# Kernel optimization log

Hardware: AMD Instinct MI355X
Metric: run time of the kernel (lower is better)

The kernel has to match this reference:

```python
import jax, jax.numpy as jnp
import numpy as np
from jax import lax

B, H, G, T = 16384, 128, 5, 12

def setup_inputs() -> dict:
    key = jax.random.key(0)
    ks = jax.random.split(key, 12)
    s = 0.05  # weight scale for numerical sanity
    return {
        "encoder_hidden": jax.random.normal(ks[0], (B, H), jnp.float32),
        "encoder_cell": jax.random.normal(ks[1], (B, H), jnp.float32),
        "last_position": jax.random.normal(ks[2], (B, 2), jnp.float32),
        "gp_w1": jax.random.normal(ks[3], (H, H), jnp.float32) * s,
        "gp_b1": jnp.zeros((H,), jnp.float32),
        "gp_w2": jax.random.normal(ks[4], (H, G * 2), jnp.float32) * s,
        "gp_b2": jnp.zeros((G * 2,), jnp.float32),
        "pr_w1": jax.random.normal(ks[5], (H, H // 2), jnp.float32) * s,
        "pr_b1": jnp.zeros((H // 2,), jnp.float32),
        "pr_w2": jax.random.normal(ks[6], (H // 2, G), jnp.float32) * s,
        "pr_b2": jnp.zeros((G,), jnp.float32),
        "w_ih": jax.random.normal(ks[7], (4, 4 * H), jnp.float32) * s,   # LSTM input weights [in=4, 4H] (i,f,g,o)
        "w_hh": jax.random.normal(ks[8], (H, 4 * H), jnp.float32) * s,   # LSTM recurrent weights [H, 4H]
        "b_ih": jnp.zeros((4 * H,), jnp.float32),
        "b_hh": jnp.zeros((4 * H,), jnp.float32),
        "ph_w": jax.random.normal(ks[9], (H, 2), jnp.float32) * s,
        "ph_b": jnp.zeros((2,), jnp.float32),
    }

def reference(encoder_hidden, encoder_cell, last_position,
              gp_w1, gp_b1, gp_w2, gp_b2,
              pr_w1, pr_b1, pr_w2, pr_b2,
              w_ih, w_hh, b_ih, b_hh, ph_w, ph_b):
    b = encoder_hidden.shape[0]
    # goal prediction: residual on last_position
    g_hid = jax.nn.relu(encoder_hidden @ gp_w1 + gp_b1)
    goals = (g_hid @ gp_w2 + gp_b2).reshape(b, G, 2) + last_position[:, None, :]  # [B,G,2]
    # goal probabilities
    p_hid = jax.nn.relu(encoder_hidden @ pr_w1 + pr_b1)
    goal_probs = jax.nn.softmax(p_hid @ pr_w2 + pr_b2, axis=-1)  # [B,G]
    # batch all goals together: leading goal dim [G,B,...]
    goals_gb = jnp.swapaxes(goals, 0, 1)                      # [G,B,2]
    h0 = jnp.broadcast_to(encoder_hidden, (G, b, H))
    c0 = jnp.broadcast_to(encoder_cell, (G, b, H))
    pos0 = jnp.broadcast_to(last_position, (G, b, 2))
    bias = b_ih + b_hh

    def step(carry, _):
        pos, h, c = carry
        x = jnp.concatenate([pos, goals_gb], axis=-1)          # [G,B,4]
        gates = x @ w_ih + h @ w_hh + bias                      # [G,B,4H]
        i, f, g, o = jnp.split(gates, 4, axis=-1)
        c_new = jax.nn.sigmoid(f) * c + jax.nn.sigmoid(i) * jnp.tanh(g)
        h_new = jax.nn.sigmoid(o) * jnp.tanh(c_new)
        pos_new = pos + (h_new @ ph_w + ph_b)                   # residual position update
        return (pos_new, h_new, c_new), pos_new

    _, path = lax.scan(step, (pos0, h0, c0), None, length=T)   # [T,G,B,2]
    predictions = jnp.transpose(path, (2, 1, 0, 3))            # [B,G,T,2]
    return predictions, goals, goal_probs
```

## Files before the change

### kernel.cpp

```cpp
#include <hip/hip_runtime.h>

#define Bn 16384
#define Hn 128
#define Gn 5
#define Tn 12

typedef __attribute__((ext_vector_type(8))) __bf16 bf16x8;
typedef __attribute__((ext_vector_type(4))) float f32x4;
typedef __attribute__((ext_vector_type(4))) unsigned int u32x4;
typedef __attribute__((ext_vector_type(2))) unsigned int u32x2;
typedef unsigned int u32;
typedef unsigned short u16;

#define MFMA(a, b, c) __builtin_amdgcn_mfma_f32_16x16x32_bf16((a), (b), (c), 0, 0, 0)

__device__ __forceinline__ u16 f2bf(float f) { return __builtin_bit_cast(u16, (__bf16)f); }
__device__ __forceinline__ u32 pk2(float a, float b) { return (u32)f2bf(a) | ((u32)f2bf(b) << 16); }

__device__ __forceinline__ int hbsw(int row, int bytein) {
    return row * 256 + ((((bytein >> 4) ^ row) & 15) << 4) + (bytein & 15);
}
__device__ __forceinline__ int pbsw(int row, int bytein) {
    return row * 128 + ((((bytein >> 4) ^ row) & 7) << 4) + (bytein & 15);
}

__global__ __launch_bounds__(256) void k_phaseA(
    const float* __restrict__ eh, const float* __restrict__ lastpos,
    const float* __restrict__ gp_w1, const float* __restrict__ gp_b1,
    const float* __restrict__ gp_w2, const float* __restrict__ gp_b2,
    const float* __restrict__ pr_w1, const float* __restrict__ pr_b1,
    const float* __restrict__ pr_w2, const float* __restrict__ pr_b2,
    float* __restrict__ goals_o, float* __restrict__ probs_o)
{
    __shared__ __align__(16) char eT[64 * 256];
    __shared__ __align__(16) char gT[64 * 256];
    __shared__ __align__(16) char pT[64 * 128];
    __shared__ float lgT[64 * 8];

    const int tid = threadIdx.x;
    const int lane = tid & 63;
    const int wv = tid >> 6;
    const int lg = lane >> 4, li = lane & 15;
    const int r0 = blockIdx.x * 64;
    const int rowbase = wv * 16;

    {
        int row = tid >> 2, seg = tid & 3;
        const float* src = eh + (size_t)(r0 + row) * Hn + seg * 32;
#pragma unroll
        for (int cc = 0; cc < 4; ++cc) {
            u32 p0 = pk2(src[cc * 8 + 0], src[cc * 8 + 1]);
            u32 p1 = pk2(src[cc * 8 + 2], src[cc * 8 + 3]);
            u32 p2 = pk2(src[cc * 8 + 4], src[cc * 8 + 5]);
            u32 p3 = pk2(src[cc * 8 + 6], src[cc * 8 + 7]);
            *(u32x4*)(eT + hbsw(row, seg * 64 + cc * 16)) = (u32x4){p0, p1, p2, p3};
        }
    }
    __syncthreads();

    bf16x8 Ae[4];
#pragma unroll
    for (int kc = 0; kc < 4; ++kc)
        Ae[kc] = *(const bf16x8*)(eT + hbsw(rowbase + li, kc * 64 + lg * 16));

#pragma unroll 1
    for (int nt = 0; nt < 8; ++nt) {
        int c1 = nt * 16 + li;
        f32x4 acc = {0.f, 0.f, 0.f, 0.f};
#pragma unroll
        for (int kc = 0; kc < 4; ++kc) {
            bf16x8 bfr;
#pragma unroll
            for (int j = 0; j < 8; ++j)
                bfr[j] = (__bf16)gp_w1[(size_t)(kc * 32 + lg * 8 + j) * Hn + c1];
            acc = MFMA(Ae[kc], bfr, acc);
        }
        float bias = gp_b1[c1];
#pragma unroll
        for (int r = 0; r < 4; ++r) {
            int row = rowbase + lg * 4 + r;
            float v = fmaxf(acc[r] + bias, 0.f);
            *(u16*)(gT + hbsw(row, c1 * 2)) = f2bf(v);
        }
    }
    __syncthreads();

    {
        bf16x8 Ag[4];
#pragma unroll
        for (int kc = 0; kc < 4; ++kc)
            Ag[kc] = *(const bf16x8*)(gT + hbsw(rowbase + li, kc * 64 + lg * 16));
        f32x4 acc = {0.f, 0.f, 0.f, 0.f};
#pragma unroll
        for (int kc = 0; kc < 4; ++kc) {
            bf16x8 bfr;
#pragma unroll
            for (int j = 0; j < 8; ++j) {
                int k = kc * 32 + lg * 8 + j;
                bfr[j] = (li < 10) ? (__bf16)gp_w2[k * 10 + li] : (__bf16)0.f;
            }
            acc = MFMA(Ag[kc], bfr, acc);
        }
        if (li < 10) {
            float b2 = gp_b2[li];
#pragma unroll
            for (int r = 0; r < 4; ++r) {
                int b = r0 + rowbase + lg * 4 + r;
                float v = acc[r] + b2 + lastpos[(size_t)b * 2 + (li & 1)];
                goals_o[(size_t)b * 10 + li] = v;
            }
        }
    }

#pragma unroll 1
    for (int nt = 0; nt < 4; ++nt) {
        int c1 = nt * 16 + li;
        f32x4 acc = {0.f, 0.f, 0.f, 0.f};
#pragma unroll
        for (int kc = 0; kc < 4; ++kc) {
            bf16x8 bfr;
#pragma unroll
            for (int j = 0; j < 8; ++j)
                bfr[j] = (__bf16)pr_w1[(size_t)(kc * 32 + lg * 8 + j) * 64 + c1];
            acc = MFMA(Ae[kc], bfr, acc);
        }
        float bias = pr_b1[c1];
#pragma unroll
        for (int r = 0; r < 4; ++r) {
            int row = rowbase + lg * 4 + r;
            float v = fmaxf(acc[r] + bias, 0.f);
            *(u16*)(pT + pbsw(row, c1 * 2)) = f2bf(v);
        }
    }
    __syncthreads();

    {
        bf16x8 Ap[2];
#pragma unroll
        for (int kc = 0; kc < 2; ++kc)
            Ap[kc] = *(const bf16x8*)(pT + pbsw(rowbase + li, kc * 64 + lg * 16));
        f32x4 acc = {0.f, 0.f, 0.f, 0.f};
#pragma unroll
        for (int kc = 0; kc < 2; ++kc) {
            bf16x8 bfr;
#pragma unroll
            for (int j = 0; j < 8; ++j) {
                int k = kc * 32 + lg * 8 + j;
                bfr[j] = (li < 5) ? (__bf16)pr_w2[k * 5 + li] : (__bf16)0.f;
            }
            acc = MFMA(Ap[kc], bfr, acc);
        }
        if (li < 5) {
            float b2 = pr_b2[li];
#pragma unroll
            for (int r = 0; r < 4; ++r) {
                int row = rowbase + lg * 4 + r;
                lgT[row * 8 + li] = acc[r] + b2;
            }
        }
    }
    __syncthreads();

    if (tid < 64) {
        int row = tid;
        float v0 = lgT[row * 8 + 0], v1 = lgT[row * 8 + 1], v2 = lgT[row * 8 + 2];
        float v3 = lgT[row * 8 + 3], v4 = lgT[row * 8 + 4];
        float mx = fmaxf(fmaxf(fmaxf(v0, v1), fmaxf(v2, v3)), v4);
        float e0 = __builtin_amdgcn_exp2f((v0 - mx) * 1.44269504f);
        float e1 = __builtin_amdgcn_exp2f((v1 - mx) * 1.44269504f);
        float e2 = __builtin_amdgcn_exp2f((v2 - mx) * 1.44269504f);
        float e3 = __builtin_amdgcn_exp2f((v3 - mx) * 1.44269504f);
        float e4 = __builtin_amdgcn_exp2f((v4 - mx) * 1.44269504f);
        float rs = __builtin_amdgcn_rcpf(e0 + e1 + e2 + e3 + e4);
        size_t ob = (size_t)(r0 + row) * 5;
        probs_o[ob + 0] = e0 * rs;
        probs_o[ob + 1] = e1 * rs;
        probs_o[ob + 2] = e2 * rs;
        probs_o[ob + 3] = e3 * rs;
        probs_o[ob + 4] = e4 * rs;
    }
}

__global__ __launch_bounds__(512) void k_lstm(
    const float* __restrict__ eh, const float* __restrict__ ec,
    const float* __restrict__ lastpos,
    const float* __restrict__ w_ih, const float* __restrict__ w_hh,
    const float* __restrict__ b_ih, const float* __restrict__ b_hh,
    const float* __restrict__ ph_w, const float* __restrict__ ph_b,
    const float* __restrict__ goals_o, float* __restrict__ preds)
{
#define MT 10
#define ROWS (MT * 16)
#define BUFB (ROWS * 256)
    __shared__ __align__(16) char hT[2][BUFB];

    const int tid = threadIdx.x;
    const int lane = tid & 63;
    const int wv = tid >> 6;
    const int lg = lane >> 4, li = lane & 15;
    const int r0 = blockIdx.x * ROWS;

    const float NL = -1.44269504f;
    const float PG = 2.88539008f;

    bf16x8 Wh[4][4];
    bf16x8 Wx[4];
#pragma unroll
    for (int gt = 0; gt < 4; ++gt) {
        const float s = (gt == 2) ? PG : NL;
        const int cg = gt * 128 + wv * 16 + li;
#pragma unroll
        for (int kc = 0; kc < 4; ++kc) {
            bf16x8 f;
#pragma unroll
            for (int j = 0; j < 8; ++j)
                f[j] = (__bf16)(w_hh[(size_t)(kc * 32 + lg * 8 + j) * 512 + cg] * s);
            Wh[gt][kc] = f;
        }
        bf16x8 fx;
#pragma unroll
        for (int j = 0; j < 8; ++j) {
            int k = lg * 8 + j;
            float v = 0.f;
            if (k < 4) v = w_ih[k * 512 + cg] * s;
            else if (k == 4) v = (b_ih[cg] + b_hh[cg]) * s;
            fx[j] = (__bf16)v;
        }
        Wx[gt] = fx;
    }

    bf16x8 php[4];
#pragma unroll
    for (int kc = 0; kc < 4; ++kc) {
        u32 w[4];
#pragma unroll
        for (int jp = 0; jp < 4; ++jp) {
            int k = kc * 32 + lg * 8 + jp * 2;
            u32 xw = pk2(ph_w[k * 2 + 0], ph_w[k * 2 + 2]);
            u32 yw = pk2(ph_w[k * 2 + 1], ph_w[k * 2 + 3]);
            w[jp] = (li == 0) ? xw : yw;
        }
        php[kc] = __builtin_bit_cast(bf16x8, (u32x4){w[0], w[1], w[2], w[3]});
    }
    const float phb0 = ph_b[0], phb1 = ph_b[1];

    u32 gpk[MT];
    float px[MT], py[MT];
#pragma unroll
    for (int m = 0; m < MT; ++m) {
        int gr = r0 + m * 16 + li;
        float2 g2 = *(const float2*)(goals_o + (size_t)gr * 2);
        gpk[m] = pk2(g2.x, g2.y);
        float2 p = *(const float2*)(lastpos + (size_t)(gr / 5) * 2);
        px[m] = p.x; py[m] = p.y;
    }

    const int ro0 = hbsw(li, 0 + lg * 16);
    const int ro1 = hbsw(li, 64 + lg * 16);
    const int ro2 = hbsw(li, 128 + lg * 16);
    const int ro3 = hbsw(li, 192 + lg * 16);
    const int wo  = hbsw(li, wv * 32 + lg * 8);

#pragma unroll
    for (int it = 0; it < 5; ++it) {
        int chunk = tid + it * 512;
        int row = chunk >> 4, seg = chunk & 15;
        const float* src = eh + (size_t)((r0 + row) / 5) * Hn + seg * 8;
        u32 p0 = pk2(src[0], src[1]);
        u32 p1 = pk2(src[2], src[3]);
        u32 p2 = pk2(src[4], src[5]);
        u32 p3 = pk2(src[6], src[7]);
        *(u32x4*)(hT[0] + hbsw(row, seg * 16)) = (u32x4){p0, p1, p2, p3};
    }

    f32x4 c[MT];
#pragma unroll
    for (int m = 0; m < MT; ++m) {
        int b = (r0 + m * 16 + li) / 5;
        float4 cv = *(const float4*)(ec + (size_t)b * Hn + wv * 16 + lg * 4);
        c[m] = (f32x4){cv.x, cv.y, cv.z, cv.w};
    }

    __syncthreads();

#pragma unroll 1
    for (int t = 0; t < Tn; ++t) {
        const char* rbp = hT[0] + (t & 1) * BUFB;
        char* wbp = hT[0] + ((t & 1) ^ 1) * BUFB;
#pragma unroll
        for (int m = 0; m < MT; ++m) {
            const int mo = m * 4096;
            bf16x8 H0 = *(const bf16x8*)(rbp + ro0 + mo);
            bf16x8 H1 = *(const bf16x8*)(rbp + ro1 + mo);
            bf16x8 H2 = *(const bf16x8*)(rbp + ro2 + mo);
            bf16x8 H3 = *(const bf16x8*)(rbp + ro3 + mo);

            f32x4 a0 = {0.f, 0.f, 0.f, 0.f}, a1 = {0.f, 0.f, 0.f, 0.f};
            f32x4 a2 = {0.f, 0.f, 0.f, 0.f}, a3 = {0.f, 0.f, 0.f, 0.f};
            a0 = MFMA(Wh[0][0], H0, a0); a1 = MFMA(Wh[1][0], H0, a1);
            a2 = MFMA(Wh[2][0], H0, a2); a3 = MFMA(Wh[3][0], H0, a3);
            a0 = MFMA(Wh[0][1], H1, a0); a1 = MFMA(Wh[1][1], H1, a1);
            a2 = MFMA(Wh[2][1], H1, a2); a3 = MFMA(Wh[3][1], H1, a3);
            a0 = MFMA(Wh[0][2], H2, a0); a1 = MFMA(Wh[1][2], H2, a1);
            a2 = MFMA(Wh[2][2], H2, a2); a3 = MFMA(Wh[3][2], H2, a3);
            a0 = MFMA(Wh[0][3], H3, a0); a1 = MFMA(Wh[1][3], H3, a1);
            a2 = MFMA(Wh[2][3], H3, a2); a3 = MFMA(Wh[3][3], H3, a3);

            if (t > 0) {
                f32x4 pacc = {0.f, 0.f, 0.f, 0.f};
                pacc = MFMA(php[0], H0, pacc);
                pacc = MFMA(php[1], H1, pacc);
                pacc = MFMA(php[2], H2, pacc);
                pacc = MFMA(php[3], H3, pacc);
                px[m] += pacc[0] + phb0;
                py[m] += pacc[1] + phb1;
                if (((m & 7) == wv) && lg == 0) {
                    size_t o = ((size_t)(r0 + m * 16 + li) * Tn + (t - 1)) * 2;
                    *(float2*)(preds + o) = make_float2(px[m], py[m]);
                }
            }

            bf16x8 xf = __builtin_bit_cast(bf16x8,
                (u32x4){pk2(px[m], py[m]), gpk[m], 0x00003F80u, 0u});
            a0 = MFMA(Wx[0], xf, a0);
            a1 = MFMA(Wx[1], xf, a1);
            a2 = MFMA(Wx[2], xf, a2);
            a3 = MFMA(Wx[3], xf, a3);

            u32 w0, w1;
            {
                float hvv[4];
#pragma unroll
                for (int r = 0; r < 4; ++r) {
                    float si = __builtin_amdgcn_rcpf(1.0f + __builtin_amdgcn_exp2f(a0[r]));
                    float sf = __builtin_amdgcn_rcpf(1.0f + __builtin_amdgcn_exp2f(a1[r]));
                    float tg = 1.0f - 2.0f * __builtin_amdgcn_rcpf(1.0f + __builtin_amdgcn_exp2f(a2[r]));
                    float so = __builtin_amdgcn_rcpf(1.0f + __builtin_amdgcn_exp2f(a3[r]));
                    float cn = sf * c[m][r] + si * tg;
                    c[m][r] = cn;
                    float tc = 1.0f - 2.0f * __builtin_amdgcn_rcpf(1.0f + __builtin_amdgcn_exp2f(PG * cn));
                    hvv[r] = so * tc;
                }
                w0 = pk2(hvv[0], hvv[1]);
                w1 = pk2(hvv[2], hvv[3]);
            }
            *(u32x2*)(wbp + wo + mo) = (u32x2){w0, w1};
        }
        __syncthreads();
    }

#pragma unroll
    for (int m = 0; m < MT; ++m) {
        if ((m & 7) != wv) continue;
        const char* rbp = hT[0];
        const int mo = m * 4096;
        bf16x8 H0 = *(const bf16x8*)(rbp + ro0 + mo);
        bf16x8 H1 = *(const bf16x8*)(rbp + ro1 + mo);
        bf16x8 H2 = *(const bf16x8*)(rbp + ro2 + mo);
        bf16x8 H3 = *(const bf16x8*)(rbp + ro3 + mo);
        f32x4 pacc = {0.f, 0.f, 0.f, 0.f};
        pacc = MFMA(php[0], H0, pacc);
        pacc = MFMA(php[1], H1, pacc);
        pacc = MFMA(php[2], H2, pacc);
        pacc = MFMA(php[3], H3, pacc);
        if (lg == 0) {
            float fx = px[m] + pacc[0] + phb0;
            float fy = py[m] + pacc[1] + phb1;
            size_t o = ((size_t)(r0 + m * 16 + li) * Tn + (Tn - 1)) * 2;
            *(float2*)(preds + o) = make_float2(fx, fy);
        }
    }
#undef MT
#undef ROWS
#undef BUFB
}

extern "C" void kernel_launch(void* const* d_in, const int* in_sizes, int n_in,
                              void* d_out, int out_size, void* d_ws, size_t ws_size,
                              hipStream_t stream)
{
    (void)in_sizes; (void)n_in; (void)out_size; (void)d_ws; (void)ws_size;
    const float* eh   = (const float*)d_in[0];
    const float* ec   = (const float*)d_in[1];
    const float* lp   = (const float*)d_in[2];
    const float* gpw1 = (const float*)d_in[3];
    const float* gpb1 = (const float*)d_in[4];
    const float* gpw2 = (const float*)d_in[5];
    const float* gpb2 = (const float*)d_in[6];
    const float* prw1 = (const float*)d_in[7];
    const float* prb1 = (const float*)d_in[8];
    const float* prw2 = (const float*)d_in[9];
    const float* prb2 = (const float*)d_in[10];
    const float* wih  = (const float*)d_in[11];
    const float* whh  = (const float*)d_in[12];
    const float* bih  = (const float*)d_in[13];
    const float* bhh  = (const float*)d_in[14];
    const float* phw  = (const float*)d_in[15];
    const float* phb  = (const float*)d_in[16];

    float* out = (float*)d_out;
    float* preds = out;
    float* goals = out + (size_t)Bn * Gn * Tn * 2;
    float* probs = out + (size_t)Bn * Gn * Tn * 2 + (size_t)Bn * Gn * 2;

    k_phaseA<<<Bn / 64, 256, 0, stream>>>(eh, lp, gpw1, gpb1, gpw2, gpb2,
                                          prw1, prb1, prw2, prb2, goals, probs);
    k_lstm<<<(Bn * Gn) / 160, 512, 0, stream>>>(eh, ec, lp, wih, whh, bih, bhh,
                                                phw, phb, goals, preds);
}
```

Baseline: 246.5 us.

## Double LSTM rows per block with single h buffer and shared position state

```diff
diff --git a/kernel.cpp b/kernel.cpp
--- a/kernel.cpp
+++ b/kernel.cpp
@@ -181,7 +181,7 @@
     }
 }
 
-__global__ __launch_bounds__(512) void k_lstm(
+__global__ __launch_bounds__(512, 2) void k_lstm(
     const float* __restrict__ eh, const float* __restrict__ ec,
     const float* __restrict__ lastpos,
     const float* __restrict__ w_ih, const float* __restrict__ w_hh,
@@ -189,10 +189,12 @@
     const float* __restrict__ ph_w, const float* __restrict__ ph_b,
     const float* __restrict__ goals_o, float* __restrict__ preds)
 {
-#define MT 10
+#define MT 20
 #define ROWS (MT * 16)
 #define BUFB (ROWS * 256)
-    __shared__ __align__(16) char hT[2][BUFB];
+    __shared__ __align__(16) char hT[BUFB];
+    __shared__ float2 posb[2][ROWS];
+    __shared__ u32 gpkT[ROWS];
 
     const int tid = threadIdx.x;
     const int lane = tid & 63;
@@ -244,17 +246,6 @@
     }
     const float phb0 = ph_b[0], phb1 = ph_b[1];
 
-    u32 gpk[MT];
-    float px[MT], py[MT];
-#pragma unroll
-    for (int m = 0; m < MT; ++m) {
-        int gr = r0 + m * 16 + li;
-        float2 g2 = *(const float2*)(goals_o + (size_t)gr * 2);
-        gpk[m] = pk2(g2.x, g2.y);
-        float2 p = *(const float2*)(lastpos + (size_t)(gr / 5) * 2);
-        px[m] = p.x; py[m] = p.y;
-    }
-
     const int ro0 = hbsw(li, 0 + lg * 16);
     const int ro1 = hbsw(li, 64 + lg * 16);
     const int ro2 = hbsw(li, 128 + lg * 16);
@@ -262,7 +253,7 @@
     const int wo  = hbsw(li, wv * 32 + lg * 8);
 
 #pragma unroll
-    for (int it = 0; it < 5; ++it) {
+    for (int it = 0; it < 10; ++it) {
         int chunk = tid + it * 512;
         int row = chunk >> 4, seg = chunk & 15;
         const float* src = eh + (size_t)((r0 + row) / 5) * Hn + seg * 8;
@@ -270,7 +261,15 @@
         u32 p1 = pk2(src[2], src[3]);
         u32 p2 = pk2(src[4], src[5]);
         u32 p3 = pk2(src[6], src[7]);
-        *(u32x4*)(hT[0] + hbsw(row, seg * 16)) = (u32x4){p0, p1, p2, p3};
+        *(u32x4*)(hT + hbsw(row, seg * 16)) = (u32x4){p0, p1, p2, p3};
+    }
+    if (tid < ROWS) {
+        int gr = r0 + tid;
+        float2 p = *(const float2*)(lastpos + (size_t)(gr / 5) * 2);
+        posb[0][tid] = p;
+        posb[1][tid] = p;
+        float2 g2 = *(const float2*)(goals_o + (size_t)gr * 2);
+        gpkT[tid] = pk2(g2.x, g2.y);
     }
 
     f32x4 c[MT];
@@ -285,15 +284,16 @@
 
 #pragma unroll 1
     for (int t = 0; t < Tn; ++t) {
-        const char* rbp = hT[0] + (t & 1) * BUFB;
-        char* wbp = hT[0] + ((t & 1) ^ 1) * BUFB;
-#pragma unroll
-        for (int m = 0; m < MT; ++m) {
+        const float2* posR = posb[t & 1];
+        float2* posW = posb[(t & 1) ^ 1];
+        u32 hnA[10], hnB[10];
+
+        auto compute = [&](int m, int i) {
             const int mo = m * 4096;
-            bf16x8 H0 = *(const bf16x8*)(rbp + ro0 + mo);
-            bf16x8 H1 = *(const bf16x8*)(rbp + ro1 + mo);
-            bf16x8 H2 = *(const bf16x8*)(rbp + ro2 + mo);
-            bf16x8 H3 = *(const bf16x8*)(rbp + ro3 + mo);
+            bf16x8 H0 = *(const bf16x8*)(hT + ro0 + mo);
+            bf16x8 H1 = *(const bf16x8*)(hT + ro1 + mo);
+            bf16x8 H2 = *(const bf16x8*)(hT + ro2 + mo);
+            bf16x8 H3 = *(const bf16x8*)(hT + ro3 + mo);
 
             f32x4 a0 = {0.f, 0.f, 0.f, 0.f}, a1 = {0.f, 0.f, 0.f, 0.f};
             f32x4 a2 = {0.f, 0.f, 0.f, 0.f}, a3 = {0.f, 0.f, 0.f, 0.f};
@@ -306,66 +306,79 @@
             a0 = MFMA(Wh[0][3], H3, a0); a1 = MFMA(Wh[1][3], H3, a1);
             a2 = MFMA(Wh[2][3], H3, a2); a3 = MFMA(Wh[3][3], H3, a3);
 
+            float2 pp = posR[m * 16 + li];
+            float pxv = pp.x, pyv = pp.y;
             if (t > 0) {
                 f32x4 pacc = {0.f, 0.f, 0.f, 0.f};
                 pacc = MFMA(php[0], H0, pacc);
                 pacc = MFMA(php[1], H1, pacc);
                 pacc = MFMA(php[2], H2, pacc);
                 pacc = MFMA(php[3], H3, pacc);
-                px[m] += pacc[0] + phb0;
-                py[m] += pacc[1] + phb1;
-                if (((m & 7) == wv) && lg == 0) {
+                pxv += pacc[0] + phb0;
+                pyv += pacc[1] + phb1;
+                if (wv == 0 && lg == 0) {
+                    posW[m * 16 + li] = make_float2(pxv, pyv);
                     size_t o = ((size_t)(r0 + m * 16 + li) * Tn + (t - 1)) * 2;
-                    *(float2*)(preds + o) = make_float2(px[m], py[m]);
+                    *(float2*)(preds + o) = make_float2(pxv, pyv);
                 }
             }
 
+            u32 gk = gpkT[m * 16 + li];
             bf16x8 xf = __builtin_bit_cast(bf16x8,
-                (u32x4){pk2(px[m], py[m]), gpk[m], 0x00003F80u, 0u});
+                (u32x4){pk2(pxv, pyv), gk, 0x00003F80u, 0u});
             a0 = MFMA(Wx[0], xf, a0);
             a1 = MFMA(Wx[1], xf, a1);
             a2 = MFMA(Wx[2], xf, a2);
             a3 = MFMA(Wx[3], xf, a3);
 
-            u32 w0, w1;
-            {
-                float hvv[4];
-#pragma unroll
-                for (int r = 0; r < 4; ++r) {
-                    float si = __builtin_amdgcn_rcpf(1.0f + __builtin_amdgcn_exp2f(a0[r]));
-                    float sf = __builtin_amdgcn_rcpf(1.0f + __builtin_amdgcn_exp2f(a1[r]));
-                    float tg = 1.0f - 2.0f * __builtin_amdgcn_rcpf(1.0f + __builtin_amdgcn_exp2f(a2[r]));
-                    float so = __builtin_amdgcn_rcpf(1.0f + __builtin_amdgcn_exp2f(a3[r]));
-                    float cn = sf * c[m][r] + si * tg;
-                    c[m][r] = cn;
-                    float tc = 1.0f - 2.0f * __builtin_amdgcn_rcpf(1.0f + __builtin_amdgcn_exp2f(PG * cn));
-                    hvv[r] = so * tc;
-                }
-                w0 = pk2(hvv[0], hvv[1]);
-                w1 = pk2(hvv[2], hvv[3]);
-            }
-            *(u32x2*)(wbp + wo + mo) = (u32x2){w0, w1};
-        }
+            float hvv[4];
+#pragma unroll
+            for (int r = 0; r < 4; ++r) {
+                float si = __builtin_amdgcn_rcpf(1.0f + __builtin_amdgcn_exp2f(a0[r]));
+                float sf = __builtin_amdgcn_rcpf(1.0f + __builtin_amdgcn_exp2f(a1[r]));
+                float tg = 1.0f - 2.0f * __builtin_amdgcn_rcpf(1.0f + __builtin_amdgcn_exp2f(a2[r]));
+                float so = __builtin_amdgcn_rcpf(1.0f + __builtin_amdgcn_exp2f(a3[r]));
+                float cn = sf * c[m][r] + si * tg;
+                c[m][r] = cn;
+                float tc = 1.0f - 2.0f * __builtin_amdgcn_rcpf(1.0f + __builtin_amdgcn_exp2f(PG * cn));
+                hvv[r] = so * tc;
+            }
+            hnA[i] = pk2(hvv[0], hvv[1]);
+            hnB[i] = pk2(hvv[2], hvv[3]);
+        };
+
+#pragma unroll
+        for (int i = 0; i < 10; ++i) compute(i, i);
+        __syncthreads();
+#pragma unroll
+        for (int i = 0; i < 10; ++i)
+            *(u32x2*)(hT + wo + i * 4096) = (u32x2){hnA[i], hnB[i]};
+#pragma unroll
+        for (int i = 0; i < 10; ++i) compute(10 + i, i);
+        __syncthreads();
+#pragma unroll
+        for (int i = 0; i < 10; ++i)
+            *(u32x2*)(hT + wo + (10 + i) * 4096) = (u32x2){hnA[i], hnB[i]};
         __syncthreads();
     }
 
 #pragma unroll
     for (int m = 0; m < MT; ++m) {
         if ((m & 7) != wv) continue;
-        const char* rbp = hT[0];
         const int mo = m * 4096;
-        bf16x8 H0 = *(const bf16x8*)(rbp + ro0 + mo);
-        bf16x8 H1 = *(const bf16x8*)(rbp + ro1 + mo);
-        bf16x8 H2 = *(const bf16x8*)(rbp + ro2 + mo);
-        bf16x8 H3 = *(const bf16x8*)(rbp + ro3 + mo);
+        bf16x8 H0 = *(const bf16x8*)(hT + ro0 + mo);
+        bf16x8 H1 = *(const bf16x8*)(hT + ro1 + mo);
+        bf16x8 H2 = *(const bf16x8*)(hT + ro2 + mo);
+        bf16x8 H3 = *(const bf16x8*)(hT + ro3 + mo);
         f32x4 pacc = {0.f, 0.f, 0.f, 0.f};
         pacc = MFMA(php[0], H0, pacc);
         pacc = MFMA(php[1], H1, pacc);
         pacc = MFMA(php[2], H2, pacc);
         pacc = MFMA(php[3], H3, pacc);
         if (lg == 0) {
-            float fx = px[m] + pacc[0] + phb0;
-            float fy = py[m] + pacc[1] + phb1;
+            float2 pp = posb[Tn & 1][m * 16 + li];
+            float fx = pp.x + pacc[0] + phb0;
+            float fy = pp.y + pacc[1] + phb1;
             size_t o = ((size_t)(r0 + m * 16 + li) * Tn + (Tn - 1)) * 2;
             *(float2*)(preds + o) = make_float2(fx, fy);
         }
@@ -405,6 +418,6 @@
 
     k_phaseA<<<Bn / 64, 256, 0, stream>>>(eh, lp, gpw1, gpb1, gpw2, gpb2,
                                           prw1, prb1, prw2, prb2, goals, probs);
-    k_lstm<<<(Bn * Gn) / 160, 512, 0, stream>>>(eh, ec, lp, wih, whh, bih, bhh,
+    k_lstm<<<(Bn * Gn) / 320, 512, 0, stream>>>(eh, ec, lp, wih, whh, bih, bhh,
                                                 phw, phb, goals, preds);
 }
```

Result: slower. 515.8 us (+109.2%).
